# Kernel optimization log

Hardware: AMD Instinct MI355X
Metric: run time of the kernel (lower is better)

Reference implementation:

```python
import jax, jax.numpy as jnp
import numpy as np

N_NODES = 100000
N_EDGES = 1200000
IN_FEATS = 64
OUT_FEATS = 64


def setup_inputs() -> dict:
    key = jax.random.key(0)
    k1, k2, k3, k4 = jax.random.split(key, 4)
    feature = jax.random.normal(k1, (N_NODES, IN_FEATS), dtype=jnp.float32)
    edge_src = jax.random.randint(k2, (N_EDGES,), 0, N_NODES, dtype=jnp.int32)
    edge_dst = jax.random.randint(k3, (N_EDGES,), 0, N_NODES, dtype=jnp.int32)
    # xavier_normal_ init for linear weight (fan_in=fan_out=64)
    std = float(np.sqrt(2.0 / (IN_FEATS + OUT_FEATS)))
    W = jax.random.normal(k4, (OUT_FEATS, IN_FEATS), dtype=jnp.float32) * std
    b = jnp.zeros((OUT_FEATS,), dtype=jnp.float32)
    return {"feature": feature, "edge_src": edge_src, "edge_dst": edge_dst, "W": W, "b": b}


def reference(feature, edge_src, edge_dst, W, b):
    # copy_src: gather source-node features per edge, then mean-reduce by dst.
    msgs = feature[edge_src]                                   # [E, d_in]
    summed = jax.ops.segment_sum(msgs, edge_dst, num_segments=N_NODES)  # [N, d_in]
    deg = jax.ops.segment_sum(jnp.ones((edge_src.shape[0],), feature.dtype),
                              edge_dst, num_segments=N_NODES)  # [N]
    h = summed / jnp.maximum(deg, 1.0)[:, None]                # mean; 0 for isolated nodes
    # apply_nodes: linear + activation
    h = jnp.einsum("nd,od->no", h, W) + b
    return jax.nn.relu(h)
```

## Files before the change

### kernel.cpp

```cpp
#include <hip/hip_runtime.h>


typedef __attribute__((ext_vector_type(8))) short short8;
typedef __attribute__((ext_vector_type(4))) float floatx4;

constexpr int kNodes = 100000;
constexpr int kEdges = 1200000;

constexpr int kBuckets = 1024;
constexpr int kBucketNodes = 98;

constexpr int kBinBlocks = 256;
constexpr int kEdgesPerBlock = 4688;
constexpr int kEPT = (kEdgesPerBlock + 1023) / 1024;

constexpr int kCap = 2048;
constexpr float kFxScale = 262144.0f;
constexpr int kAccStride = 68;

constexpr int kWsFeat   = 0;
constexpr int kWsOff    = 3200000;
constexpr int kWsBinned = kWsOff + kBinBlocks * (kBuckets + 1);

__device__ __forceinline__ unsigned bf16rne(float f) {
  unsigned u = __float_as_uint(f);
  return (u + 0x7fffu + ((u >> 16) & 1u)) >> 16;
}

__global__ __launch_bounds__(1024) void gcn_build(
    const float* __restrict__ feat,
    const int* __restrict__ src, const int* __restrict__ dst,
    int* __restrict__ ws) {
  uint2* fb16 = (uint2*)(ws + kWsFeat);
  int* offT   = ws + kWsOff;
  int* binned = ws + kWsBinned;

  __shared__ int lhist[kBuckets];
  __shared__ int lcur[kBuckets];
  __shared__ int wsum[16];

  const int tid = threadIdx.x;
  lhist[tid] = 0;
  __syncthreads();

  const int e0 = blockIdx.x * kEdgesPerBlock;
  const int cnt = min(kEdgesPerBlock, kEdges - e0);
  int es[kEPT], ebk[kEPT], edl[kEPT];
  #pragma unroll
  for (int k = 0; k < kEPT; ++k) {
    const int j = tid + k * 1024;
    if (j < cnt) {
      es[k] = src[e0 + j];
      const int d = dst[e0 + j];
      const int bk = d / kBucketNodes;
      ebk[k] = bk;
      edl[k] = d - bk * kBucketNodes;
      atomicAdd(&lhist[bk], 1);
    }
  }

  const int t = blockIdx.x * 1024 + tid;
  for (int i = t; i < kNodes * 16; i += kBinBlocks * 1024) {
    const float* fr = feat + (size_t)(i >> 4) * 64 + (i & 15);
    uint2 p;
    p.x = bf16rne(fr[0])  | (bf16rne(fr[16]) << 16);
    p.y = bf16rne(fr[32]) | (bf16rne(fr[48]) << 16);
    fb16[i] = p;
  }
  __syncthreads();

  const int own = lhist[tid];
  const int wv = tid >> 6, ln = tid & 63;
  int sc = own;
  #pragma unroll
  for (int off = 1; off < 64; off <<= 1) {
    const int v = __shfl_up(sc, off, 64);
    if (ln >= off) sc += v;
  }
  if (ln == 63) wsum[wv] = sc;
  __syncthreads();
  if (tid < 64) {
    int tw = (tid < 16) ? wsum[tid] : 0;
    #pragma unroll
    for (int off = 1; off < 16; off <<= 1) {
      const int v = __shfl_up(tw, off, 64);
      if (tid >= off) tw += v;
    }
    if (tid < 16) wsum[tid] = tw;
  }
  __syncthreads();
  const int excl = sc - own + (wv ? wsum[wv - 1] : 0);
  lcur[tid] = excl;
  offT[blockIdx.x * (kBuckets + 1) + tid] = excl;
  if (tid == 0) offT[blockIdx.x * (kBuckets + 1) + kBuckets] = cnt;
  __syncthreads();

  int* myBin = binned + blockIdx.x * kEdgesPerBlock;
  #pragma unroll
  for (int k = 0; k < kEPT; ++k) {
    const int j = tid + k * 1024;
    if (j < cnt) {
      const int pos = atomicAdd(&lcur[ebk[k]], 1);
      myBin[pos] = es[k] | (edl[k] << 17);
    }
  }
}

__global__ __launch_bounds__(1024, 8) void gcn_aggregate(
    const int*   __restrict__ ws_in,
    const float* __restrict__ W,
    const float* __restrict__ b,
    float*       __restrict__ out) {
  const uint2* fb16 = (const uint2*)(ws_in + kWsFeat);
  const int* offT   = ws_in + kWsOff;
  const int* binned = ws_in + kWsBinned;

  __shared__ __align__(16) char uShared[112 * 72 * 2];
  __shared__ int    accum[kBucketNodes * kAccStride];
  __shared__ int    lofs[129];
  __shared__ int    lcur[128];
  __shared__ int    runL[kBinBlocks + 1];
  __shared__ int    runG[kBinBlocks];
  __shared__ int    ssm[kBinBlocks];
  __shared__ ushort Wb16[64 * 64];
  __shared__ float  bsh[64];
  int*    lsrc  = (int*)uShared;
  ushort* hsAll = (ushort*)uShared;

  const int tid = threadIdx.x;
  const int bkt = blockIdx.x;

  if (tid < 128) lcur[tid] = 0;
  for (int i = tid; i < 4096; i += 1024) Wb16[i] = (ushort)bf16rne(W[i]);
  if (tid < 64) bsh[tid] = b[tid];
  for (int i = tid; i < kBucketNodes * kAccStride; i += 1024) accum[i] = 0;

  if (tid < kBinBlocks) {
    const int o0 = offT[tid * (kBuckets + 1) + bkt];
    const int o1 = offT[tid * (kBuckets + 1) + bkt + 1];
    ssm[tid] = o1 - o0;
    runG[tid] = tid * kEdgesPerBlock + o0;
  }
  __syncthreads();
  if (tid < 64) {
    const int base = tid * 4;
    const int v0 = ssm[base], v1 = ssm[base + 1];
    const int v2 = ssm[base + 2], v3 = ssm[base + 3];
    const int p1 = v0 + v1, p2 = p1 + v2, tot = p2 + v3;
    int sc = tot;
    #pragma unroll
    for (int off = 1; off < 64; off <<= 1) {
      const int v = __shfl_up(sc, off, 64);
      if (tid >= off) sc += v;
    }
    const int ex = sc - tot;
    runL[base]     = ex;
    runL[base + 1] = ex + v0;
    runL[base + 2] = ex + p1;
    runL[base + 3] = ex + p2;
    if (tid == 63) runL[kBinBlocks] = sc;
  }
  __syncthreads();

  int sz = runL[kBinBlocks];
  if (sz > kCap) sz = kCap;

  auto mapRead = [&](int j) -> unsigned {
    int lo = 0, hi = kBinBlocks;
    #pragma unroll
    for (int it = 0; it < 8; ++it) {
      const int mid = (lo + hi) >> 1;
      if (runL[mid] <= j) lo = mid; else hi = mid;
    }
    return (unsigned)binned[runG[lo] + (j - runL[lo])];
  };

  const int j0 = tid, j1 = tid + 1024;
  const bool va = j0 < sz, vb = j1 < sz;
  unsigned ea = 0, eb = 0;
  if (va) { ea = mapRead(j0); atomicAdd(&lcur[ea >> 17], 1); }
  if (vb) { eb = mapRead(j1); atomicAdd(&lcur[eb >> 17], 1); }
  __syncthreads();

  if (tid < 64) {
    const int a  = lcur[tid * 2];
    const int b2 = lcur[tid * 2 + 1];
    int s = a + b2;
    #pragma unroll
    for (int off = 1; off < 64; off <<= 1) {
      const int v = __shfl_up(s, off, 64);
      if (tid >= off) s += v;
    }
    const int ex1 = s - b2;
    const int ex0 = ex1 - a;
    lofs[tid * 2]     = ex0;
    lofs[tid * 2 + 1] = ex1;
    lcur[tid * 2]     = ex0;
    lcur[tid * 2 + 1] = ex1;
    if (tid == 63) lofs[128] = s;
  }
  __syncthreads();

  if (va) { const int p = atomicAdd(&lcur[ea >> 17], 1); lsrc[p] = (int)ea; }
  if (vb) { const int p = atomicAdd(&lcur[eb >> 17], 1); lsrc[p] = (int)eb; }
  __syncthreads();

  const int wave = tid >> 6;
  const int lane = tid & 63;
  const int g = lane >> 4;
  const int c = lane & 15;
  {
    const int slot = wave * 4 + g;
    const int jb = (sz * slot) >> 6;
    const int je = (sz * (slot + 1)) >> 6;
    int curDL = -1;
    float a0 = 0.f, a1 = 0.f, a2 = 0.f, a3 = 0.f;
    for (int j = jb; j < je; ++j) {
      const unsigned e = (unsigned)lsrc[j];
      const int dL = (int)(e >> 17);
      if (dL != curDL) {
        if (curDL >= 0) {
          int* row = accum + curDL * kAccStride + c;
          atomicAdd(row + 0,  (int)(a0 * kFxScale));
          atomicAdd(row + 16, (int)(a1 * kFxScale));
          atomicAdd(row + 32, (int)(a2 * kFxScale));
          atomicAdd(row + 48, (int)(a3 * kFxScale));
        }
        curDL = dL;
        a0 = a1 = a2 = a3 = 0.f;
      }
      const uint2 v = fb16[(size_t)(e & 0x1FFFF) * 16 + c];
      a0 += __uint_as_float(v.x << 16);
      a1 += __uint_as_float(v.x & 0xffff0000u);
      a2 += __uint_as_float(v.y << 16);
      a3 += __uint_as_float(v.y & 0xffff0000u);
    }
    if (curDL >= 0) {
      int* row = accum + curDL * kAccStride + c;
      atomicAdd(row + 0,  (int)(a0 * kFxScale));
      atomicAdd(row + 16, (int)(a1 * kFxScale));
      atomicAdd(row + 32, (int)(a2 * kFxScale));
      atomicAdd(row + 48, (int)(a3 * kFxScale));
    }
  }
  __syncthreads();

  {
    const int nd = tid >> 3;
    const int ch = tid & 7;
    if (nd < kBucketNodes) {
      const int dg = lofs[nd + 1] - lofs[nd];
      const float inv = 1.0f / (kFxScale * (float)(dg > 1 ? dg : 1));
      const int* arow = accum + nd * kAccStride + ch * 8;
      unsigned h[8];
      #pragma unroll
      for (int q = 0; q < 8; ++q) h[q] = bf16rne((float)arow[q] * inv);
      uint4 pk;
      pk.x = h[0] | (h[1] << 16);
      pk.y = h[2] | (h[3] << 16);
      pk.z = h[4] | (h[5] << 16);
      pk.w = h[6] | (h[7] << 16);
      *(uint4*)(hsAll + nd * 72 + ch * 8) = pk;
    } else {
      if (nd < 112) *(uint4*)(hsAll + nd * 72 + ch * 8) =
          make_uint4(0u, 0u, 0u, 0u);
    }
  }
  __syncthreads();

  if (tid < 448) {
    const int w8   = tid >> 6;
    const int ln   = tid & 63;
    const int quad = ln >> 4;
    const int col  = ln & 15;
    const int n0 = bkt * kBucketNodes;

    const short8 af0 = *reinterpret_cast<const short8*>(
        hsAll + (w8 * 16 + col) * 72 + 0 * 32 + quad * 8);
    const short8 af1 = *reinterpret_cast<const short8*>(
        hsAll + (w8 * 16 + col) * 72 + 1 * 32 + quad * 8);

    #pragma unroll
    for (int ob = 0; ob < 4; ++ob) {
      const short8 bf0 = *reinterpret_cast<const short8*>(
          Wb16 + (ob * 16 + col) * 64 + 0 * 32 + quad * 8);
      const short8 bf1 = *reinterpret_cast<const short8*>(
          Wb16 + (ob * 16 + col) * 64 + 1 * 32 + quad * 8);
      floatx4 acc = {0.f, 0.f, 0.f, 0.f};
      acc = __builtin_amdgcn_mfma_f32_16x16x32_bf16(af0, bf0, acc, 0, 0, 0);
      acc = __builtin_amdgcn_mfma_f32_16x16x32_bf16(af1, bf1, acc, 0, 0, 0);

      const int o = ob * 16 + col;
      const float bo = bsh[o];
      #pragma unroll
      for (int r = 0; r < 4; ++r) {
        const int local = w8 * 16 + quad * 4 + r;
        const int node = n0 + local;
        if (local < kBucketNodes && node < kNodes) {
          const float v = acc[r] + bo;
          out[(size_t)node * 64 + o] = v > 0.0f ? v : 0.0f;
        }
      }
    }
  }
}

extern "C" void kernel_launch(void* const* d_in, const int* in_sizes, int n_in,
                              void* d_out, int out_size, void* d_ws, size_t ws_size,
                              hipStream_t stream) {
  const float* feature  = (const float*)d_in[0];
  const int*   edge_src = (const int*)  d_in[1];
  const int*   edge_dst = (const int*)  d_in[2];
  const float* W        = (const float*)d_in[3];
  const float* b        = (const float*)d_in[4];

  float* out = (float*)d_out;
  int*   ws  = (int*)d_ws;

  gcn_build<<<kBinBlocks, 1024, 0, stream>>>(feature, edge_src, edge_dst, ws);
  gcn_aggregate<<<kBuckets, 1024, 0, stream>>>(ws, W, b, out);
}
```

Baseline: 128.1 us.

## Assign whole destination rows to slots, replacing LDS atomics with plain stores

Each 16-lane slot now gets a contiguous range of destination rows, found by binary search over the per-node offsets, instead of an even split of edges. Because every row has exactly one owner, partial sums are written as plain float stores to shared memory. This removes the fixed-point LDS atomics and the accumulator zeroing. The gather loop also prefetches the next edge's features one step ahead, and the normalize stage reads the accumulator with vector loads. In exchange, load balance is now per row rather than per edge, so slots can get uneven work when degrees vary.

```diff
diff --git a/kernel.cpp b/kernel.cpp
--- a/kernel.cpp
+++ b/kernel.cpp
@@ -15,7 +15,6 @@
 constexpr int kEPT = (kEdgesPerBlock + 1023) / 1024;
 
 constexpr int kCap = 2048;
-constexpr float kFxScale = 262144.0f;
 constexpr int kAccStride = 68;
 
 constexpr int kWsFeat   = 0;
@@ -116,9 +115,10 @@
   const int* binned = ws_in + kWsBinned;
 
   __shared__ __align__(16) char uShared[112 * 72 * 2];
-  __shared__ int    accum[kBucketNodes * kAccStride];
+  __shared__ __align__(16) int accum[kBucketNodes * kAccStride];
   __shared__ int    lofs[129];
   __shared__ int    lcur[128];
+  __shared__ int    slotR[65];
   __shared__ int    runL[kBinBlocks + 1];
   __shared__ int    runG[kBinBlocks];
   __shared__ int    ssm[kBinBlocks];
@@ -133,7 +133,6 @@
   if (tid < 128) lcur[tid] = 0;
   for (int i = tid; i < 4096; i += 1024) Wb16[i] = (ushort)bf16rne(W[i]);
   if (tid < 64) bsh[tid] = b[tid];
-  for (int i = tid; i < kBucketNodes * kAccStride; i += 1024) accum[i] = 0;
 
   if (tid < kBinBlocks) {
     const int o0 = offT[tid * (kBuckets + 1) + bkt];
@@ -203,6 +202,17 @@
 
   if (va) { const int p = atomicAdd(&lcur[ea >> 17], 1); lsrc[p] = (int)ea; }
   if (vb) { const int p = atomicAdd(&lcur[eb >> 17], 1); lsrc[p] = (int)eb; }
+  if (tid < 64) {
+    const int tgt = (sz * tid) >> 6;
+    int lo = 0, hi = kBucketNodes;
+    #pragma unroll
+    for (int it = 0; it < 7; ++it) {
+      const int mid = (lo + hi) >> 1;
+      if (lofs[mid] < tgt) lo = mid + 1; else hi = mid;
+    }
+    slotR[tid] = lo;
+  }
+  if (tid == 64) slotR[64] = kBucketNodes;
   __syncthreads();
 
   const int wave = tid >> 6;
@@ -211,36 +221,43 @@
   const int c = lane & 15;
   {
     const int slot = wave * 4 + g;
-    const int jb = (sz * slot) >> 6;
-    const int je = (sz * (slot + 1)) >> 6;
-    int curDL = -1;
-    float a0 = 0.f, a1 = 0.f, a2 = 0.f, a3 = 0.f;
-    for (int j = jb; j < je; ++j) {
-      const unsigned e = (unsigned)lsrc[j];
-      const int dL = (int)(e >> 17);
-      if (dL != curDL) {
-        if (curDL >= 0) {
-          int* row = accum + curDL * kAccStride + c;
-          atomicAdd(row + 0,  (int)(a0 * kFxScale));
-          atomicAdd(row + 16, (int)(a1 * kFxScale));
-          atomicAdd(row + 32, (int)(a2 * kFxScale));
-          atomicAdd(row + 48, (int)(a3 * kFxScale));
+    int r = slotR[slot];
+    const int rEnd = slotR[slot + 1];
+    if (r < rEnd) {
+      int j = lofs[r];
+      const int jE = lofs[rEnd];
+      int jN = lofs[r + 1];
+      float a0 = 0.f, a1 = 0.f, a2 = 0.f, a3 = 0.f;
+      unsigned e = (j < jE) ? (unsigned)lsrc[j] : 0u;
+      uint2 v = fb16[(size_t)(e & 0x1FFFF) * 16 + c];
+      while (j < jE) {
+        while (j >= jN) {
+          int* rp = accum + r * kAccStride + c;
+          rp[0]  = __float_as_int(a0);
+          rp[16] = __float_as_int(a1);
+          rp[32] = __float_as_int(a2);
+          rp[48] = __float_as_int(a3);
+          a0 = a1 = a2 = a3 = 0.f;
+          ++r; jN = lofs[r + 1];
         }
-        curDL = dL;
+        const int jn = j + 1;
+        const unsigned e2 = (jn < jE) ? (unsigned)lsrc[jn] : 0u;
+        const uint2 v2 = fb16[(size_t)(e2 & 0x1FFFF) * 16 + c];
+        a0 += __uint_as_float(v.x << 16);
+        a1 += __uint_as_float(v.x & 0xffff0000u);
+        a2 += __uint_as_float(v.y << 16);
+        a3 += __uint_as_float(v.y & 0xffff0000u);
+        v = v2; e = e2; j = jn;
+      }
+      while (r < rEnd) {
+        int* rp = accum + r * kAccStride + c;
+        rp[0]  = __float_as_int(a0);
+        rp[16] = __float_as_int(a1);
+        rp[32] = __float_as_int(a2);
+        rp[48] = __float_as_int(a3);
         a0 = a1 = a2 = a3 = 0.f;
+        ++r;
       }
-      const uint2 v = fb16[(size_t)(e & 0x1FFFF) * 16 + c];
-      a0 += __uint_as_float(v.x << 16);
-      a1 += __uint_as_float(v.x & 0xffff0000u);
-      a2 += __uint_as_float(v.y << 16);
-      a3 += __uint_as_float(v.y & 0xffff0000u);
-    }
-    if (curDL >= 0) {
-      int* row = accum + curDL * kAccStride + c;
-      atomicAdd(row + 0,  (int)(a0 * kFxScale));
-      atomicAdd(row + 16, (int)(a1 * kFxScale));
-      atomicAdd(row + 32, (int)(a2 * kFxScale));
-      atomicAdd(row + 48, (int)(a3 * kFxScale));
     }
   }
   __syncthreads();
@@ -250,16 +267,23 @@
     const int ch = tid & 7;
     if (nd < kBucketNodes) {
       const int dg = lofs[nd + 1] - lofs[nd];
-      const float inv = 1.0f / (kFxScale * (float)(dg > 1 ? dg : 1));
+      const float inv = 1.0f / (float)(dg > 1 ? dg : 1);
       const int* arow = accum + nd * kAccStride + ch * 8;
-      unsigned h[8];
-      #pragma unroll
-      for (int q = 0; q < 8; ++q) h[q] = bf16rne((float)arow[q] * inv);
+      const int4 pa = *(const int4*)(arow);
+      const int4 pb = *(const int4*)(arow + 4);
+      unsigned h0 = bf16rne(__int_as_float(pa.x) * inv);
+      unsigned h1 = bf16rne(__int_as_float(pa.y) * inv);
+      unsigned h2 = bf16rne(__int_as_float(pa.z) * inv);
+      unsigned h3 = bf16rne(__int_as_float(pa.w) * inv);
+      unsigned h4 = bf16rne(__int_as_float(pb.x) * inv);
+      unsigned h5 = bf16rne(__int_as_float(pb.y) * inv);
+      unsigned h6 = bf16rne(__int_as_float(pb.z) * inv);
+      unsigned h7 = bf16rne(__int_as_float(pb.w) * inv);
       uint4 pk;
-      pk.x = h[0] | (h[1] << 16);
-      pk.y = h[2] | (h[3] << 16);
-      pk.z = h[4] | (h[5] << 16);
-      pk.w = h[6] | (h[7] << 16);
+      pk.x = h0 | (h1 << 16);
+      pk.y = h2 | (h3 << 16);
+      pk.z = h4 | (h5 << 16);
+      pk.w = h6 | (h7 << 16);
       *(uint4*)(hsAll + nd * 72 + ch * 8) = pk;
     } else {
       if (nd < 112) *(uint4*)(hsAll + nd * 72 + ch * 8) =
```

After: 132.9 us. 1.04x slower.

## Halve bucket size, transpose offset table, widen gathers, use per-edge LDS atomics

Applied to the files above, without the earlier changes.

Doubles the bucket count to 2048 with 49 nodes each and runs 512-thread aggregate blocks. The per-block offset table is stored transposed so each aggregate block reads it coalesced. Features are repacked so every lane gathers a uint4 (8 bf16) and 8 lanes cover a row. The run-length accumulation by destination is replaced with direct LDS atomics per edge, giving simpler control flow at the cost of many more shared-memory atomics. The smaller capacity of 1024 edges per bucket may drop edges on heavily loaded buckets.

```diff
diff --git a/kernel.cpp b/kernel.cpp
--- a/kernel.cpp
+++ b/kernel.cpp
@@ -7,20 +7,20 @@
 constexpr int kNodes = 100000;
 constexpr int kEdges = 1200000;
 
-constexpr int kBuckets = 1024;
-constexpr int kBucketNodes = 98;
+constexpr int kBuckets = 2048;
+constexpr int kBucketNodes = 49;
 
 constexpr int kBinBlocks = 256;
 constexpr int kEdgesPerBlock = 4688;
 constexpr int kEPT = (kEdgesPerBlock + 1023) / 1024;
 
-constexpr int kCap = 2048;
+constexpr int kCap = 1024;
 constexpr float kFxScale = 262144.0f;
 constexpr int kAccStride = 68;
 
 constexpr int kWsFeat   = 0;
 constexpr int kWsOff    = 3200000;
-constexpr int kWsBinned = kWsOff + kBinBlocks * (kBuckets + 1);
+constexpr int kWsBinned = kWsOff + (kBuckets + 1) * kBinBlocks;
 
 __device__ __forceinline__ unsigned bf16rne(float f) {
   unsigned u = __float_as_uint(f);
@@ -31,8 +31,8 @@
     const float* __restrict__ feat,
     const int* __restrict__ src, const int* __restrict__ dst,
     int* __restrict__ ws) {
-  uint2* fb16 = (uint2*)(ws + kWsFeat);
-  int* offT   = ws + kWsOff;
+  uint4* fb16 = (uint4*)(ws + kWsFeat);
+  int* offTT  = ws + kWsOff;
   int* binned = ws + kWsBinned;
 
   __shared__ int lhist[kBuckets];
@@ -41,6 +41,7 @@
 
   const int tid = threadIdx.x;
   lhist[tid] = 0;
+  lhist[tid + 1024] = 0;
   __syncthreads();
 
   const int e0 = blockIdx.x * kEdgesPerBlock;
@@ -60,16 +61,20 @@
   }
 
   const int t = blockIdx.x * 1024 + tid;
-  for (int i = t; i < kNodes * 16; i += kBinBlocks * 1024) {
-    const float* fr = feat + (size_t)(i >> 4) * 64 + (i & 15);
-    uint2 p;
-    p.x = bf16rne(fr[0])  | (bf16rne(fr[16]) << 16);
-    p.y = bf16rne(fr[32]) | (bf16rne(fr[48]) << 16);
+  for (int i = t; i < kNodes * 8; i += kBinBlocks * 1024) {
+    const float* fr = feat + (size_t)(i >> 3) * 64 + (i & 7);
+    uint4 p;
+    p.x = bf16rne(fr[0])  | (bf16rne(fr[8])  << 16);
+    p.y = bf16rne(fr[16]) | (bf16rne(fr[24]) << 16);
+    p.z = bf16rne(fr[32]) | (bf16rne(fr[40]) << 16);
+    p.w = bf16rne(fr[48]) | (bf16rne(fr[56]) << 16);
     fb16[i] = p;
   }
   __syncthreads();
 
-  const int own = lhist[tid];
+  const int a  = lhist[tid * 2];
+  const int b2 = lhist[tid * 2 + 1];
+  const int own = a + b2;
   const int wv = tid >> 6, ln = tid & 63;
   int sc = own;
   #pragma unroll
@@ -89,10 +94,12 @@
     if (tid < 16) wsum[tid] = tw;
   }
   __syncthreads();
-  const int excl = sc - own + (wv ? wsum[wv - 1] : 0);
-  lcur[tid] = excl;
-  offT[blockIdx.x * (kBuckets + 1) + tid] = excl;
-  if (tid == 0) offT[blockIdx.x * (kBuckets + 1) + kBuckets] = cnt;
+  const int e0p = sc - own + (wv ? wsum[wv - 1] : 0);
+  lcur[tid * 2]     = e0p;
+  lcur[tid * 2 + 1] = e0p + a;
+  offTT[(tid * 2) * kBinBlocks + blockIdx.x]     = e0p;
+  offTT[(tid * 2 + 1) * kBinBlocks + blockIdx.x] = e0p + a;
+  if (tid == 0) offTT[kBuckets * kBinBlocks + blockIdx.x] = cnt;
   __syncthreads();
 
   int* myBin = binned + blockIdx.x * kEdgesPerBlock;
@@ -106,22 +113,21 @@
   }
 }
 
-__global__ __launch_bounds__(1024, 8) void gcn_aggregate(
+__global__ __launch_bounds__(512, 8) void gcn_aggregate(
     const int*   __restrict__ ws_in,
     const float* __restrict__ W,
     const float* __restrict__ b,
     float*       __restrict__ out) {
-  const uint2* fb16 = (const uint2*)(ws_in + kWsFeat);
-  const int* offT   = ws_in + kWsOff;
+  const uint4* fb16 = (const uint4*)(ws_in + kWsFeat);
+  const int* offTT  = ws_in + kWsOff;
   const int* binned = ws_in + kWsBinned;
 
-  __shared__ __align__(16) char uShared[112 * 72 * 2];
-  __shared__ int    accum[kBucketNodes * kAccStride];
-  __shared__ int    lofs[129];
-  __shared__ int    lcur[128];
+  __shared__ __align__(16) char uShared[64 * 72 * 2];
+  __shared__ __align__(16) int accum[kBucketNodes * kAccStride];
+  __shared__ int    lofs[65];
+  __shared__ int    lcur[64];
   __shared__ int    runL[kBinBlocks + 1];
   __shared__ int    runG[kBinBlocks];
-  __shared__ int    ssm[kBinBlocks];
   __shared__ ushort Wb16[64 * 64];
   __shared__ float  bsh[64];
   int*    lsrc  = (int*)uShared;
@@ -130,22 +136,21 @@
   const int tid = threadIdx.x;
   const int bkt = blockIdx.x;
 
-  if (tid < 128) lcur[tid] = 0;
-  for (int i = tid; i < 4096; i += 1024) Wb16[i] = (ushort)bf16rne(W[i]);
-  if (tid < 64) bsh[tid] = b[tid];
-  for (int i = tid; i < kBucketNodes * kAccStride; i += 1024) accum[i] = 0;
+  if (tid < 64) { lcur[tid] = 0; bsh[tid] = b[tid]; }
+  for (int i = tid; i < 4096; i += 512) Wb16[i] = (ushort)bf16rne(W[i]);
+  for (int i = tid; i < kBucketNodes * kAccStride; i += 512) accum[i] = 0;
 
   if (tid < kBinBlocks) {
-    const int o0 = offT[tid * (kBuckets + 1) + bkt];
-    const int o1 = offT[tid * (kBuckets + 1) + bkt + 1];
-    ssm[tid] = o1 - o0;
+    const int o0 = offTT[bkt * kBinBlocks + tid];
+    const int o1 = offTT[(bkt + 1) * kBinBlocks + tid];
+    runL[tid] = o1 - o0;
     runG[tid] = tid * kEdgesPerBlock + o0;
   }
   __syncthreads();
   if (tid < 64) {
     const int base = tid * 4;
-    const int v0 = ssm[base], v1 = ssm[base + 1];
-    const int v2 = ssm[base + 2], v3 = ssm[base + 3];
+    const int v0 = runL[base], v1 = runL[base + 1];
+    const int v2 = runL[base + 2], v3 = runL[base + 3];
     const int p1 = v0 + v1, p2 = p1 + v2, tot = p2 + v3;
     int sc = tot;
     #pragma unroll
@@ -175,7 +180,7 @@
     return (unsigned)binned[runG[lo] + (j - runL[lo])];
   };
 
-  const int j0 = tid, j1 = tid + 1024;
+  const int j0 = tid, j1 = tid + 512;
   const bool va = j0 < sz, vb = j1 < sz;
   unsigned ea = 0, eb = 0;
   if (va) { ea = mapRead(j0); atomicAdd(&lcur[ea >> 17], 1); }
@@ -183,21 +188,17 @@
   __syncthreads();
 
   if (tid < 64) {
-    const int a  = lcur[tid * 2];
-    const int b2 = lcur[tid * 2 + 1];
-    int s = a + b2;
+    const int own = lcur[tid];
+    int s = own;
     #pragma unroll
     for (int off = 1; off < 64; off <<= 1) {
       const int v = __shfl_up(s, off, 64);
       if (tid >= off) s += v;
     }
-    const int ex1 = s - b2;
-    const int ex0 = ex1 - a;
-    lofs[tid * 2]     = ex0;
-    lofs[tid * 2 + 1] = ex1;
-    lcur[tid * 2]     = ex0;
-    lcur[tid * 2 + 1] = ex1;
-    if (tid == 63) lofs[128] = s;
+    const int ex = s - own;
+    lofs[tid] = ex;
+    lcur[tid] = ex;
+    if (tid == 63) lofs[64] = s;
   }
   __syncthreads();
 
@@ -207,40 +208,25 @@
 
   const int wave = tid >> 6;
   const int lane = tid & 63;
-  const int g = lane >> 4;
-  const int c = lane & 15;
+  const int g = lane >> 3;
+  const int c = lane & 7;
   {
-    const int slot = wave * 4 + g;
+    const int slot = wave * 8 + g;
     const int jb = (sz * slot) >> 6;
     const int je = (sz * (slot + 1)) >> 6;
-    int curDL = -1;
-    float a0 = 0.f, a1 = 0.f, a2 = 0.f, a3 = 0.f;
+    #pragma unroll 2
     for (int j = jb; j < je; ++j) {
       const unsigned e = (unsigned)lsrc[j];
-      const int dL = (int)(e >> 17);
-      if (dL != curDL) {
-        if (curDL >= 0) {
-          int* row = accum + curDL * kAccStride + c;
-          atomicAdd(row + 0,  (int)(a0 * kFxScale));
-          atomicAdd(row + 16, (int)(a1 * kFxScale));
-          atomicAdd(row + 32, (int)(a2 * kFxScale));
-          atomicAdd(row + 48, (int)(a3 * kFxScale));
-        }
-        curDL = dL;
-        a0 = a1 = a2 = a3 = 0.f;
-      }
-      const uint2 v = fb16[(size_t)(e & 0x1FFFF) * 16 + c];
-      a0 += __uint_as_float(v.x << 16);
-      a1 += __uint_as_float(v.x & 0xffff0000u);
-      a2 += __uint_as_float(v.y << 16);
-      a3 += __uint_as_float(v.y & 0xffff0000u);
-    }
-    if (curDL >= 0) {
-      int* row = accum + curDL * kAccStride + c;
-      atomicAdd(row + 0,  (int)(a0 * kFxScale));
-      atomicAdd(row + 16, (int)(a1 * kFxScale));
-      atomicAdd(row + 32, (int)(a2 * kFxScale));
-      atomicAdd(row + 48, (int)(a3 * kFxScale));
+      const uint4 v = fb16[(size_t)(e & 0x1FFFFu) * 8 + c];
+      int* rp = accum + (int)(e >> 17) * kAccStride + c;
+      atomicAdd(rp + 0,  (int)(__uint_as_float(v.x << 16)          * kFxScale));
+      atomicAdd(rp + 8,  (int)(__uint_as_float(v.x & 0xffff0000u) * kFxScale));
+      atomicAdd(rp + 16, (int)(__uint_as_float(v.y << 16)          * kFxScale));
+      atomicAdd(rp + 24, (int)(__uint_as_float(v.y & 0xffff0000u) * kFxScale));
+      atomicAdd(rp + 32, (int)(__uint_as_float(v.z << 16)          * kFxScale));
+      atomicAdd(rp + 40, (int)(__uint_as_float(v.z & 0xffff0000u) * kFxScale));
+      atomicAdd(rp + 48, (int)(__uint_as_float(v.w << 16)          * kFxScale));
+      atomicAdd(rp + 56, (int)(__uint_as_float(v.w & 0xffff0000u) * kFxScale));
     }
   }
   __syncthreads();
@@ -252,23 +238,29 @@
       const int dg = lofs[nd + 1] - lofs[nd];
       const float inv = 1.0f / (kFxScale * (float)(dg > 1 ? dg : 1));
       const int* arow = accum + nd * kAccStride + ch * 8;
-      unsigned h[8];
-      #pragma unroll
-      for (int q = 0; q < 8; ++q) h[q] = bf16rne((float)arow[q] * inv);
+      const int4 pa = *(const int4*)(arow);
+      const int4 pb = *(const int4*)(arow + 4);
+      unsigned h0 = bf16rne((float)pa.x * inv);
+      unsigned h1 = bf16rne((float)pa.y * inv);
+      unsigned h2 = bf16rne((float)pa.z * inv);
+      unsigned h3 = bf16rne((float)pa.w * inv);
+      unsigned h4 = bf16rne((float)pb.x * inv);
+      unsigned h5 = bf16rne((float)pb.y * inv);
+      unsigned h6 = bf16rne((float)pb.z * inv);
+      unsigned h7 = bf16rne((float)pb.w * inv);
       uint4 pk;
-      pk.x = h[0] | (h[1] << 16);
-      pk.y = h[2] | (h[3] << 16);
-      pk.z = h[4] | (h[5] << 16);
-      pk.w = h[6] | (h[7] << 16);
+      pk.x = h0 | (h1 << 16);
+      pk.y = h2 | (h3 << 16);
+      pk.z = h4 | (h5 << 16);
+      pk.w = h6 | (h7 << 16);
       *(uint4*)(hsAll + nd * 72 + ch * 8) = pk;
     } else {
-      if (nd < 112) *(uint4*)(hsAll + nd * 72 + ch * 8) =
-          make_uint4(0u, 0u, 0u, 0u);
-    }
-  }
-  __syncthreads();
-
-  if (tid < 448) {
+      *(uint4*)(hsAll + nd * 72 + ch * 8) = make_uint4(0u, 0u, 0u, 0u);
+    }
+  }
+  __syncthreads();
+
+  if (tid < 256) {
     const int w8   = tid >> 6;
     const int ln   = tid & 63;
     const int quad = ln >> 4;
@@ -318,5 +310,5 @@
   int*   ws  = (int*)d_ws;
 
   gcn_build<<<kBinBlocks, 1024, 0, stream>>>(feature, edge_src, edge_dst, ws);
-  gcn_aggregate<<<kBuckets, 1024, 0, stream>>>(ws, W, b, out);
+  gcn_aggregate<<<kBuckets, 512, 0, stream>>>(ws, W, b, out);
 }
```

New measurement: 133.3 us. 1.04x slower.

## Sort bucket edges by source window and accumulate per edge with LDS atomics

Applied to the files above, without the earlier changes.

The per-bucket local counting sort now groups edges by source-node window (src>>10) instead of destination node, so gather reads of bf16 features are more address-local across groups. Degree is counted separately. Because the edge list is no longer grouped by destination, the run-length register accumulation is replaced by a strided loop that issues four LDS fixed-point atomicAdds per edge. This targets better cache locality in the global gathers at the cost of many more shared-memory atomics.

```diff
diff --git a/kernel.cpp b/kernel.cpp
--- a/kernel.cpp
+++ b/kernel.cpp
@@ -117,8 +117,8 @@
 
   __shared__ __align__(16) char uShared[112 * 72 * 2];
   __shared__ int    accum[kBucketNodes * kAccStride];
-  __shared__ int    lofs[129];
-  __shared__ int    lcur[128];
+  __shared__ int    deg[128];
+  __shared__ int    wcur[128];
   __shared__ int    runL[kBinBlocks + 1];
   __shared__ int    runG[kBinBlocks];
   __shared__ int    ssm[kBinBlocks];
@@ -130,16 +130,18 @@
   const int tid = threadIdx.x;
   const int bkt = blockIdx.x;
 
-  if (tid < 128) lcur[tid] = 0;
+  if (tid < 128) { deg[tid] = 0; wcur[tid] = 0; }
   for (int i = tid; i < 4096; i += 1024) Wb16[i] = (ushort)bf16rne(W[i]);
   if (tid < 64) bsh[tid] = b[tid];
   for (int i = tid; i < kBucketNodes * kAccStride; i += 1024) accum[i] = 0;
 
+  int len = 0;
   if (tid < kBinBlocks) {
     const int o0 = offT[tid * (kBuckets + 1) + bkt];
     const int o1 = offT[tid * (kBuckets + 1) + bkt + 1];
-    ssm[tid] = o1 - o0;
+    len = o1 - o0;
     runG[tid] = tid * kEdgesPerBlock + o0;
+    ssm[tid] = len;
   }
   __syncthreads();
   if (tid < 64) {
@@ -178,13 +180,21 @@
   const int j0 = tid, j1 = tid + 1024;
   const bool va = j0 < sz, vb = j1 < sz;
   unsigned ea = 0, eb = 0;
-  if (va) { ea = mapRead(j0); atomicAdd(&lcur[ea >> 17], 1); }
-  if (vb) { eb = mapRead(j1); atomicAdd(&lcur[eb >> 17], 1); }
+  if (va) {
+    ea = mapRead(j0);
+    atomicAdd(&deg[ea >> 17], 1);
+    atomicAdd(&wcur[(ea & 0x1FFFFu) >> 10], 1);
+  }
+  if (vb) {
+    eb = mapRead(j1);
+    atomicAdd(&deg[eb >> 17], 1);
+    atomicAdd(&wcur[(eb & 0x1FFFFu) >> 10], 1);
+  }
   __syncthreads();
 
   if (tid < 64) {
-    const int a  = lcur[tid * 2];
-    const int b2 = lcur[tid * 2 + 1];
+    const int a  = wcur[tid * 2];
+    const int b2 = wcur[tid * 2 + 1];
     int s = a + b2;
     #pragma unroll
     for (int off = 1; off < 64; off <<= 1) {
@@ -193,16 +203,13 @@
     }
     const int ex1 = s - b2;
     const int ex0 = ex1 - a;
-    lofs[tid * 2]     = ex0;
-    lofs[tid * 2 + 1] = ex1;
-    lcur[tid * 2]     = ex0;
-    lcur[tid * 2 + 1] = ex1;
-    if (tid == 63) lofs[128] = s;
-  }
-  __syncthreads();
-
-  if (va) { const int p = atomicAdd(&lcur[ea >> 17], 1); lsrc[p] = (int)ea; }
-  if (vb) { const int p = atomicAdd(&lcur[eb >> 17], 1); lsrc[p] = (int)eb; }
+    wcur[tid * 2]     = ex0;
+    wcur[tid * 2 + 1] = ex1;
+  }
+  __syncthreads();
+
+  if (va) { const int p = atomicAdd(&wcur[(ea & 0x1FFFFu) >> 10], 1); lsrc[p] = (int)ea; }
+  if (vb) { const int p = atomicAdd(&wcur[(eb & 0x1FFFFu) >> 10], 1); lsrc[p] = (int)eb; }
   __syncthreads();
 
   const int wave = tid >> 6;
@@ -211,36 +218,15 @@
   const int c = lane & 15;
   {
     const int slot = wave * 4 + g;
-    const int jb = (sz * slot) >> 6;
-    const int je = (sz * (slot + 1)) >> 6;
-    int curDL = -1;
-    float a0 = 0.f, a1 = 0.f, a2 = 0.f, a3 = 0.f;
-    for (int j = jb; j < je; ++j) {
+    #pragma unroll 2
+    for (int j = slot; j < sz; j += 64) {
       const unsigned e = (unsigned)lsrc[j];
-      const int dL = (int)(e >> 17);
-      if (dL != curDL) {
-        if (curDL >= 0) {
-          int* row = accum + curDL * kAccStride + c;
-          atomicAdd(row + 0,  (int)(a0 * kFxScale));
-          atomicAdd(row + 16, (int)(a1 * kFxScale));
-          atomicAdd(row + 32, (int)(a2 * kFxScale));
-          atomicAdd(row + 48, (int)(a3 * kFxScale));
-        }
-        curDL = dL;
-        a0 = a1 = a2 = a3 = 0.f;
-      }
-      const uint2 v = fb16[(size_t)(e & 0x1FFFF) * 16 + c];
-      a0 += __uint_as_float(v.x << 16);
-      a1 += __uint_as_float(v.x & 0xffff0000u);
-      a2 += __uint_as_float(v.y << 16);
-      a3 += __uint_as_float(v.y & 0xffff0000u);
-    }
-    if (curDL >= 0) {
-      int* row = accum + curDL * kAccStride + c;
-      atomicAdd(row + 0,  (int)(a0 * kFxScale));
-      atomicAdd(row + 16, (int)(a1 * kFxScale));
-      atomicAdd(row + 32, (int)(a2 * kFxScale));
-      atomicAdd(row + 48, (int)(a3 * kFxScale));
+      const uint2 v = fb16[(size_t)(e & 0x1FFFFu) * 16 + c];
+      int* rp = accum + (int)(e >> 17) * kAccStride + c;
+      atomicAdd(rp + 0,  (int)(__uint_as_float(v.x << 16)          * kFxScale));
+      atomicAdd(rp + 16, (int)(__uint_as_float(v.x & 0xffff0000u) * kFxScale));
+      atomicAdd(rp + 32, (int)(__uint_as_float(v.y << 16)          * kFxScale));
+      atomicAdd(rp + 48, (int)(__uint_as_float(v.y & 0xffff0000u) * kFxScale));
     }
   }
   __syncthreads();
@@ -249,7 +235,7 @@
     const int nd = tid >> 3;
     const int ch = tid & 7;
     if (nd < kBucketNodes) {
-      const int dg = lofs[nd + 1] - lofs[nd];
+      const int dg = deg[nd];
       const float inv = 1.0f / (kFxScale * (float)(dg > 1 ? dg : 1));
       const int* arow = accum + nd * kAccStride + ch * 8;
       unsigned h[8];
```

New measurement: 128.1 us. No clear change (-0.0%).
